# Kernel tuning notes

Hardware: AMD Instinct MI355X
Metric: run time of the kernel (lower is better)

Reference implementation:

```python
import jax, jax.numpy as jnp
import numpy as np


def setup_inputs() -> dict:
    key = jax.random.key(0)
    x = jax.random.normal(key, (256, 512, 1024), dtype=jnp.float32)
    return {"x": x}


def reference(x) -> jnp.ndarray:
    # Per-row (first dim) fake-quantization to int8 range, dequant, then ReLU.
    # Original torch code loops over rows; here we vectorize with keepdims reductions.
    red_axes = tuple(range(1, x.ndim))
    M = jnp.max(x, axis=red_axes, keepdims=True)  # per-row max (detached in original)
    m = jnp.min(x, axis=red_axes, keepdims=True)  # per-row min (detached in original)
    rng = M - m
    # quantize: round(254*(x-m)/(M-m) - 127) / 1000   (the /1000, *1000 pair is kept for bit-faithfulness)
    q = jnp.round(254.0 * (x - m) / rng - 127.0) / 1000.0
    # dequantize: (1000*q + 127) * (M-m)/254 + m
    deq = (1000.0 * q + 127.0) * rng / 254.0 + m
    return jax.nn.relu(deq)
```

## Files before the change

### kernel.cpp

```cpp
#include <hip/hip_runtime.h>
#include <math.h>

constexpr int ROWS    = 256;
constexpr int ROWLEN  = 512 * 1024;
constexpr int CHUNKS  = 32;
constexpr int BLOCK   = 256;
constexpr int ROWF4   = ROWLEN / 4;
constexpr int CHUNKF4 = ROWF4 / CHUNKS;
constexpr int F4_PER_THREAD = CHUNKF4 / BLOCK;

__global__ __launch_bounds__(BLOCK) void rowminmax_partial(
    const float4* __restrict__ x,
    float* __restrict__ pmin, float* __restrict__ pmax) {
  const int bid   = blockIdx.x;
  const int row   = bid >> 5;
  const int chunk = bid & (CHUNKS - 1);
  const float4* p = x + (size_t)row * ROWF4 + (size_t)chunk * CHUNKF4;

  float vmin = INFINITY, vmax = -INFINITY;
#pragma unroll
  for (int i = 0; i < F4_PER_THREAD; ++i) {
    float4 v = p[threadIdx.x + i * BLOCK];
    vmin = fminf(vmin, fminf(fminf(v.x, v.y), fminf(v.z, v.w)));
    vmax = fmaxf(vmax, fmaxf(fmaxf(v.x, v.y), fmaxf(v.z, v.w)));
  }

#pragma unroll
  for (int off = 32; off > 0; off >>= 1) {
    vmin = fminf(vmin, __shfl_xor(vmin, off, 64));
    vmax = fmaxf(vmax, __shfl_xor(vmax, off, 64));
  }

  __shared__ float smin[BLOCK / 64], smax[BLOCK / 64];
  const int wave = threadIdx.x >> 6;
  const int lane = threadIdx.x & 63;
  if (lane == 0) { smin[wave] = vmin; smax[wave] = vmax; }
  __syncthreads();
  if (threadIdx.x == 0) {
    float a = smin[0], b = smax[0];
#pragma unroll
    for (int w = 1; w < BLOCK / 64; ++w) {
      a = fminf(a, smin[w]);
      b = fmaxf(b, smax[w]);
    }
    pmin[bid] = a;
    pmax[bid] = b;
  }
}

__global__ __launch_bounds__(BLOCK) void quant_relu(
    const float4* __restrict__ x, float4* __restrict__ out,
    const float* __restrict__ pmin, const float* __restrict__ pmax) {
  const int bid   = (int)gridDim.x - 1 - (int)blockIdx.x;
  const int row   = bid >> 5;
  const int chunk = bid & (CHUNKS - 1);

  float m = INFINITY, M = -INFINITY;
#pragma unroll
  for (int i = 0; i < CHUNKS; ++i) {
    m = fminf(m, pmin[row * CHUNKS + i]);
    M = fmaxf(M, pmax[row * CHUNKS + i]);
  }
  const float rng   = M - m;
  const float scale = 254.0f / rng;
  const float step  = rng / 254.0f;

  const float4* p = x   + (size_t)row * ROWF4 + (size_t)chunk * CHUNKF4;
  float4*       q = out + (size_t)row * ROWF4 + (size_t)chunk * CHUNKF4;

#pragma unroll 4
  for (int i = 0; i < F4_PER_THREAD; ++i) {
    float4 v = p[threadIdx.x + i * BLOCK];
    float4 o;
    o.x = fmaxf(fmaf(rintf(fmaf(v.x - m, scale, -127.0f)) + 127.0f, step, m), 0.0f);
    o.y = fmaxf(fmaf(rintf(fmaf(v.y - m, scale, -127.0f)) + 127.0f, step, m), 0.0f);
    o.z = fmaxf(fmaf(rintf(fmaf(v.z - m, scale, -127.0f)) + 127.0f, step, m), 0.0f);
    o.w = fmaxf(fmaf(rintf(fmaf(v.w - m, scale, -127.0f)) + 127.0f, step, m), 0.0f);
    q[threadIdx.x + i * BLOCK] = o;
  }
}

extern "C" void kernel_launch(void* const* d_in, const int* in_sizes, int n_in,
                              void* d_out, int out_size, void* d_ws, size_t ws_size,
                              hipStream_t stream) {
  const float4* x   = (const float4*)d_in[0];
  float4*       out = (float4*)d_out;
  float*        pmin = (float*)d_ws;
  float*        pmax = pmin + ROWS * CHUNKS;

  rowminmax_partial<<<ROWS * CHUNKS, BLOCK, 0, stream>>>((const float4*)x, pmin, pmax);
  quant_relu<<<ROWS * CHUNKS, BLOCK, 0, stream>>>(x, out, pmin, pmax);
}
```

Before: 944.0 us.

## Process rows in cache-sized groups and use nontemporal output stores

Splits the two-pass min/max and quantize work into groups of 32 rows launched alternately. Each group's input slice can stay in the last-level cache for the second read, so it does not have to be refetched from HBM. Output stores become nontemporal so the written data does not evict the input. The cost is more kernel launches and smaller grids per launch.

Measured after the change: 919.5 us. 1.03x faster.

```diff
diff --git a/kernel.cpp b/kernel.cpp
--- a/kernel.cpp
+++ b/kernel.cpp
@@ -9,12 +9,17 @@
 constexpr int CHUNKF4 = ROWF4 / CHUNKS;
 constexpr int F4_PER_THREAD = CHUNKF4 / BLOCK;
 
+typedef float natf4 __attribute__((ext_vector_type(4)));
+
+constexpr int GROUP_ROWS = 32;
+constexpr int NGROUPS    = ROWS / GROUP_ROWS;
+
 __global__ __launch_bounds__(BLOCK) void rowminmax_partial(
     const float4* __restrict__ x,
-    float* __restrict__ pmin, float* __restrict__ pmax) {
-  const int bid   = blockIdx.x;
-  const int row   = bid >> 5;
-  const int chunk = bid & (CHUNKS - 1);
+    float* __restrict__ pmin, float* __restrict__ pmax, int row0) {
+  const int row   = row0 + (blockIdx.x >> 5);
+  const int chunk = blockIdx.x & (CHUNKS - 1);
+  const int pidx  = row * CHUNKS + chunk;
   const float4* p = x + (size_t)row * ROWF4 + (size_t)chunk * CHUNKF4;
 
   float vmin = INFINITY, vmax = -INFINITY;
@@ -43,17 +48,16 @@
       a = fminf(a, smin[w]);
       b = fmaxf(b, smax[w]);
     }
-    pmin[bid] = a;
-    pmax[bid] = b;
+    pmin[pidx] = a;
+    pmax[pidx] = b;
   }
 }
 
 __global__ __launch_bounds__(BLOCK) void quant_relu(
     const float4* __restrict__ x, float4* __restrict__ out,
-    const float* __restrict__ pmin, const float* __restrict__ pmax) {
-  const int bid   = (int)gridDim.x - 1 - (int)blockIdx.x;
-  const int row   = bid >> 5;
-  const int chunk = bid & (CHUNKS - 1);
+    const float* __restrict__ pmin, const float* __restrict__ pmax, int row0) {
+  const int row   = row0 + (blockIdx.x >> 5);
+  const int chunk = blockIdx.x & (CHUNKS - 1);
 
   float m = INFINITY, M = -INFINITY;
 #pragma unroll
@@ -71,12 +75,12 @@
 #pragma unroll 4
   for (int i = 0; i < F4_PER_THREAD; ++i) {
     float4 v = p[threadIdx.x + i * BLOCK];
-    float4 o;
+    natf4 o;
     o.x = fmaxf(fmaf(rintf(fmaf(v.x - m, scale, -127.0f)) + 127.0f, step, m), 0.0f);
     o.y = fmaxf(fmaf(rintf(fmaf(v.y - m, scale, -127.0f)) + 127.0f, step, m), 0.0f);
     o.z = fmaxf(fmaf(rintf(fmaf(v.z - m, scale, -127.0f)) + 127.0f, step, m), 0.0f);
     o.w = fmaxf(fmaf(rintf(fmaf(v.w - m, scale, -127.0f)) + 127.0f, step, m), 0.0f);
-    q[threadIdx.x + i * BLOCK] = o;
+    __builtin_nontemporal_store(o, (natf4*)&q[threadIdx.x + i * BLOCK]);
   }
 }
 
@@ -88,6 +92,9 @@
   float*        pmin = (float*)d_ws;
   float*        pmax = pmin + ROWS * CHUNKS;
 
-  rowminmax_partial<<<ROWS * CHUNKS, BLOCK, 0, stream>>>((const float4*)x, pmin, pmax);
-  quant_relu<<<ROWS * CHUNKS, BLOCK, 0, stream>>>(x, out, pmin, pmax);
+  for (int g = 0; g < NGROUPS; ++g) {
+    const int row0 = g * GROUP_ROWS;
+    rowminmax_partial<<<GROUP_ROWS * CHUNKS, BLOCK, 0, stream>>>(x, pmin, pmax, row0);
+    quant_relu<<<GROUP_ROWS * CHUNKS, BLOCK, 0, stream>>>(x, out, pmin, pmax, row0);
+  }
 }
```
